# Performance work log

Hardware: AMD Instinct MI355X
Metric: run time of the kernel (lower is better)

Reference implementation:

```python
import jax, jax.numpy as jnp
import numpy as np

N_CENTER = 4000
N_NEIGH = 16
N_FEAT = 64
N_ATOMS = 20000
N_SPECIES = 8
COS_EPS = 1e-8  # torch cosine_similarity eps


def setup_inputs() -> dict:
    key = jax.random.key(0)
    k1, k2, k3, k4, k5, k6 = jax.random.split(key, 6)
    atom_i_idx = jax.random.randint(k1, (N_CENTER,), 0, N_ATOMS, dtype=jnp.int32)
    atom_j_idx = jax.random.randint(k2, (N_CENTER, N_NEIGH), 0, N_ATOMS, dtype=jnp.int32)
    # physical distances in [0.5, 4.5) Angstrom to avoid near-zero divisions
    dist_ij = jax.random.uniform(k3, (N_CENTER, N_NEIGH), dtype=jnp.float32) * 4.0 + 0.5
    atoms_xyz = jax.random.normal(k4, (N_ATOMS, 3), dtype=jnp.float32) * 5.0
    atoms_long = jax.random.randint(k5, (N_ATOMS, 2), 0, N_SPECIES, dtype=jnp.int32)
    embed_table = jax.random.normal(k6, (N_SPECIES, N_FEAT), dtype=jnp.float32)
    return {
        "nNeigh": N_NEIGH,
        "atom_i_idx": atom_i_idx,
        "atom_j_idx": atom_j_idx,
        "dist_ij": dist_ij,
        "atoms_xyz": atoms_xyz,
        "atoms_long": atoms_long,
        "embed_table": embed_table,
    }


def reference(nNeigh, atom_i_idx, atom_j_idx, dist_ij, atoms_xyz, atoms_long, embed_table):
    C = atom_i_idx.shape[0]
    N = nNeigh
    F = embed_table.shape[1]

    # --- triple geometry ---
    xyz_i = atoms_xyz[atom_i_idx][:, None, None, :]          # [C,1,1,3]
    xyz_j = atoms_xyz[atom_j_idx]                            # [C,N,3]
    vec_ij = xyz_j[:, :, None, :] - xyz_i                    # [C,N,1,3]
    vec_ik = xyz_j[:, None, :, :] - xyz_i                    # [C,1,N,3]

    dot = jnp.sum(vec_ij * vec_ik, axis=-1)                  # [C,N,N]
    norm_j = jnp.linalg.norm(vec_ij, axis=-1)                # [C,N,1]
    norm_k = jnp.linalg.norm(vec_ik, axis=-1)                # [C,1,N]
    cos = dot / (jnp.maximum(norm_j, COS_EPS) * jnp.maximum(norm_k, COS_EPS))
    ang = jnp.arccos(cos * 0.9999)                           # [C,N,N]

    d_ij = dist_ij[:, :, None, None]                         # [C,N,1,1]
    d_ik = dist_ij[:, None, :, None]                         # [C,1,N,1]

    # --- embeddings ---
    emb_i = embed_table[atoms_long[atom_i_idx, 1]]           # [C,F]
    emb_j = embed_table[atoms_long[atom_j_idx, 1]]           # [C,N,F]

    shp1 = (C, N, N, 1)
    shpF = (C, N, N, F)
    ang_desc = jnp.concatenate(
        (
            jnp.broadcast_to(d_ij, shp1),
            jnp.broadcast_to(d_ik, shp1),
            ang[..., None],
            jnp.broadcast_to(emb_i[:, None, None, :], shpF),
            jnp.broadcast_to(emb_j[:, :, None, :] / d_ij, shpF),
            jnp.broadcast_to(emb_j[:, None, :, :] / d_ik, shpF),
        ),
        axis=-1,
    )                                                         # [C,N,N,3+3F]

    # off-diagonal (j != k) triples, static index set
    jj, kk = np.nonzero(~np.eye(N, dtype=bool))
    ang_desc = ang_desc[:, jj, kk, :]                         # [C,N*(N-1),3+3F]
    return atom_i_idx.reshape(-1), ang_desc
```

## Files before the change

kernel.cpp:

```cpp
#include <hip/hip_runtime.h>
#include <math.h>

#define NNEI   16
#define NFEAT  64
#define NPAIR  240
#define ROWW   195
#define PER_C  (NPAIR * ROWW)
#define COS_EPS 1e-8f

typedef float f32x4 __attribute__((ext_vector_type(4)));

__device__ __host__ __forceinline__ int swz(int w) { return w ^ ((w >> 5) & 3); }

__global__ __launch_bounds__(256) void build_offtable(unsigned short* __restrict__ tab) {
    const int t = blockIdx.x * 256 + threadIdx.x;
    if (t >= PER_C) return;
    const unsigned p = (unsigned)t / 195u;
    const int s = t - (int)p * 195;
    const unsigned ju = p / 15u;
    const int j = (int)ju;
    const int r = (int)(p - ju * 15u);
    const int k = r + (r >= j);
    const int off =
          (s >= 131) ? (336 + (k << 6) + (s - 131))
        : (s >= 67)  ? (336 + (j << 6) + (s - 67))
        : (s >= 3)   ? (269 + s)
        : (s == 2)   ? ((j << 4) + k)
        : (s == 1)   ? (256 + k)
                     : (256 + j);
    tab[t] = (unsigned short)swz(off);
}

__global__ __launch_bounds__(256) void angdesc_kernel(
    const int*   __restrict__ atom_i_idx,
    const int*   __restrict__ atom_j_idx,
    const float* __restrict__ dist_ij,
    const float* __restrict__ atoms_xyz,
    const int*   __restrict__ atoms_long,
    const float* __restrict__ embed_table,
    const unsigned short* __restrict__ tab,
    float*       __restrict__ out0,
    float*       __restrict__ out1)
{
    __shared__ float s_lds[1360];
    __shared__ float s_vec[NNEI][3];
    __shared__ float s_nrm[NNEI];
    __shared__ float s_invd[NNEI];
    __shared__ int   s_spec[NNEI];

    const int c   = blockIdx.x;
    const int tid = threadIdx.x;
    const int ii  = atom_i_idx[c];

    if (tid == 0) out0[c] = (float)ii;

    const float xi = atoms_xyz[ii * 3 + 0];
    const float yi = atoms_xyz[ii * 3 + 1];
    const float zi = atoms_xyz[ii * 3 + 2];

    if (tid < NNEI) {
        const int jn = atom_j_idx[c * NNEI + tid];
        const float vx = atoms_xyz[jn * 3 + 0] - xi;
        const float vy = atoms_xyz[jn * 3 + 1] - yi;
        const float vz = atoms_xyz[jn * 3 + 2] - zi;
        s_vec[tid][0] = vx; s_vec[tid][1] = vy; s_vec[tid][2] = vz;
        s_nrm[tid]  = sqrtf(vx * vx + vy * vy + vz * vz);
        const float d = dist_ij[c * NNEI + tid];
        s_lds[swz(256 + tid)] = d;
        s_invd[tid] = 1.0f / d;
        s_spec[tid] = atoms_long[jn * 2 + 1];
    } else if (tid >= 64 && tid < 128) {
        const int f = tid - 64;
        const int speci = atoms_long[ii * 2 + 1];
        s_lds[swz(272 + f)] = embed_table[speci * NFEAT + f];
    }
    __syncthreads();

    {
        const int j = tid >> 4, k = tid & 15;
        const float dot = s_vec[j][0] * s_vec[k][0]
                        + s_vec[j][1] * s_vec[k][1]
                        + s_vec[j][2] * s_vec[k][2];
        const float nj = fmaxf(s_nrm[j], COS_EPS);
        const float nk = fmaxf(s_nrm[k], COS_EPS);
        const float cosv = dot / (nj * nk);
        s_lds[swz(tid)] = acosf(cosv * 0.9999f);
    }
    for (int e = tid; e < NNEI * NFEAT; e += 256) {
        const int n = e >> 6, f = e & 63;
        s_lds[swz(336 + e)] = embed_table[s_spec[n] * NFEAT + f] * s_invd[n];
    }
    __syncthreads();

    f32x4* __restrict__ dst4 = (f32x4*)(out1 + (size_t)c * PER_C);
    const ushort4* __restrict__ tab4 = (const ushort4*)tab;
    #pragma unroll 4
    for (int q = tid; q < PER_C / 4; q += 256) {
        const ushort4 o = tab4[q];
        f32x4 v;
        v.x = s_lds[o.x];
        v.y = s_lds[o.y];
        v.z = s_lds[o.z];
        v.w = s_lds[o.w];
        __builtin_nontemporal_store(v, dst4 + q);
    }
}

extern "C" void kernel_launch(void* const* d_in, const int* in_sizes, int n_in,
                              void* d_out, int out_size, void* d_ws, size_t ws_size,
                              hipStream_t stream) {
    const int*   atom_i_idx  = (const int*)  d_in[1];
    const int*   atom_j_idx  = (const int*)  d_in[2];
    const float* dist_ij     = (const float*)d_in[3];
    const float* atoms_xyz   = (const float*)d_in[4];
    const int*   atoms_long  = (const int*)  d_in[5];
    const float* embed_table = (const float*)d_in[6];

    const int C = in_sizes[1];
    float* out  = (float*)d_out;
    unsigned short* tab = (unsigned short*)d_ws;

    build_offtable<<<(PER_C + 255) / 256, 256, 0, stream>>>(tab);
    angdesc_kernel<<<C, 256, 0, stream>>>(atom_i_idx, atom_j_idx, dist_ij,
                                          atoms_xyz, atoms_long, embed_table,
                                          tab, out, out + C);
}
```

Before: 754.6 us.

## Make angular descriptor kernel persistent with multiple centers per block

Launches a fixed grid of 512 blocks, each processing 8 consecutive centers, with an XCD-interleaved block-to-work mapping. This amortizes block launch overhead and reuses the table across centers. It adds a fallback path that computes gather offsets inline when no workspace is available. In exchange it reduces the number of resident blocks and serializes each block's setup phase against its streaming stores, which may lower the parallelism available to hide latency.

Result: no change. 758.6 us (+0.5%).

```diff
diff --git a/kernel.cpp b/kernel.cpp
--- a/kernel.cpp
+++ b/kernel.cpp
@@ -6,7 +6,10 @@
 #define NPAIR  240
 #define ROWW   195
 #define PER_C  (NPAIR * ROWW)
+#define IMG    1360
 #define COS_EPS 1e-8f
+#define CPB    8
+#define NBLK   512
 
 typedef float f32x4 __attribute__((ext_vector_type(4)));
 
@@ -31,7 +34,23 @@
     tab[t] = (unsigned short)swz(off);
 }
 
-__global__ __launch_bounds__(256) void angdesc_kernel(
+__device__ __forceinline__ int off_of(int p, int s) {
+    const unsigned ju = (unsigned)p / 15u;
+    const int j = (int)ju;
+    const int r = p - (int)ju * 15;
+    const int k = r + (r >= j);
+    int off;
+    if      (s >= 131) off = 336 + (k << 6) + (s - 131);
+    else if (s >= 67)  off = 336 + (j << 6) + (s - 67);
+    else if (s >= 3)   off = 269 + s;
+    else if (s == 2)   off = (j << 4) + k;
+    else if (s == 1)   off = 256 + k;
+    else               off = 256 + j;
+    return swz(off);
+}
+
+template <bool USE_TAB>
+__global__ __launch_bounds__(256) void angdesc_persist(
     const int*   __restrict__ atom_i_idx,
     const int*   __restrict__ atom_j_idx,
     const float* __restrict__ dist_ij,
@@ -40,69 +59,92 @@
     const float* __restrict__ embed_table,
     const unsigned short* __restrict__ tab,
     float*       __restrict__ out0,
-    float*       __restrict__ out1)
+    float*       __restrict__ out1,
+    int C)
 {
-    __shared__ float s_lds[1360];
+    alignas(16) __shared__ float s_lds[IMG];
     __shared__ float s_vec[NNEI][3];
     __shared__ float s_nrm[NNEI];
     __shared__ float s_invd[NNEI];
     __shared__ int   s_spec[NNEI];
 
-    const int c   = blockIdx.x;
     const int tid = threadIdx.x;
-    const int ii  = atom_i_idx[c];
+    const int b = blockIdx.x;
+    const int logical = ((b & 7) << 6) + (b >> 3);
+    const int c0 = logical * CPB;
 
-    if (tid == 0) out0[c] = (float)ii;
+    for (int c = c0; c < c0 + CPB && c < C; ++c) {
+        __syncthreads();
 
-    const float xi = atoms_xyz[ii * 3 + 0];
-    const float yi = atoms_xyz[ii * 3 + 1];
-    const float zi = atoms_xyz[ii * 3 + 2];
+        const int ii = atom_i_idx[c];
+        if (tid == 0) out0[c] = (float)ii;
+        const float xi = atoms_xyz[ii * 3 + 0];
+        const float yi = atoms_xyz[ii * 3 + 1];
+        const float zi = atoms_xyz[ii * 3 + 2];
 
-    if (tid < NNEI) {
-        const int jn = atom_j_idx[c * NNEI + tid];
-        const float vx = atoms_xyz[jn * 3 + 0] - xi;
-        const float vy = atoms_xyz[jn * 3 + 1] - yi;
-        const float vz = atoms_xyz[jn * 3 + 2] - zi;
-        s_vec[tid][0] = vx; s_vec[tid][1] = vy; s_vec[tid][2] = vz;
-        s_nrm[tid]  = sqrtf(vx * vx + vy * vy + vz * vz);
-        const float d = dist_ij[c * NNEI + tid];
-        s_lds[swz(256 + tid)] = d;
-        s_invd[tid] = 1.0f / d;
-        s_spec[tid] = atoms_long[jn * 2 + 1];
-    } else if (tid >= 64 && tid < 128) {
-        const int f = tid - 64;
-        const int speci = atoms_long[ii * 2 + 1];
-        s_lds[swz(272 + f)] = embed_table[speci * NFEAT + f];
-    }
-    __syncthreads();
+        if (tid < NNEI) {
+            const int jn = atom_j_idx[c * NNEI + tid];
+            const float vx = atoms_xyz[jn * 3 + 0] - xi;
+            const float vy = atoms_xyz[jn * 3 + 1] - yi;
+            const float vz = atoms_xyz[jn * 3 + 2] - zi;
+            s_vec[tid][0] = vx; s_vec[tid][1] = vy; s_vec[tid][2] = vz;
+            s_nrm[tid]  = sqrtf(vx * vx + vy * vy + vz * vz);
+            const float d = dist_ij[c * NNEI + tid];
+            s_lds[swz(256 + tid)] = d;
+            s_invd[tid] = 1.0f / d;
+            s_spec[tid] = atoms_long[jn * 2 + 1];
+        } else if (tid >= 64 && tid < 128) {
+            const int f = tid - 64;
+            const int speci = atoms_long[ii * 2 + 1];
+            s_lds[swz(272 + f)] = embed_table[speci * NFEAT + f];
+        }
+        __syncthreads();
 
-    {
-        const int j = tid >> 4, k = tid & 15;
-        const float dot = s_vec[j][0] * s_vec[k][0]
-                        + s_vec[j][1] * s_vec[k][1]
-                        + s_vec[j][2] * s_vec[k][2];
-        const float nj = fmaxf(s_nrm[j], COS_EPS);
-        const float nk = fmaxf(s_nrm[k], COS_EPS);
-        const float cosv = dot / (nj * nk);
-        s_lds[swz(tid)] = acosf(cosv * 0.9999f);
-    }
-    for (int e = tid; e < NNEI * NFEAT; e += 256) {
-        const int n = e >> 6, f = e & 63;
-        s_lds[swz(336 + e)] = embed_table[s_spec[n] * NFEAT + f] * s_invd[n];
-    }
-    __syncthreads();
+        {
+            const int j = tid >> 4, k = tid & 15;
+            const float dot = s_vec[j][0] * s_vec[k][0]
+                            + s_vec[j][1] * s_vec[k][1]
+                            + s_vec[j][2] * s_vec[k][2];
+            const float nj = fmaxf(s_nrm[j], COS_EPS);
+            const float nk = fmaxf(s_nrm[k], COS_EPS);
+            s_lds[swz(tid)] = acosf((dot / (nj * nk)) * 0.9999f);
+        }
+        for (int e = tid; e < NNEI * NFEAT; e += 256) {
+            const int n = e >> 6, f = e & 63;
+            s_lds[swz(336 + e)] = embed_table[s_spec[n] * NFEAT + f] * s_invd[n];
+        }
+        __syncthreads();
 
-    f32x4* __restrict__ dst4 = (f32x4*)(out1 + (size_t)c * PER_C);
-    const ushort4* __restrict__ tab4 = (const ushort4*)tab;
-    #pragma unroll 4
-    for (int q = tid; q < PER_C / 4; q += 256) {
-        const ushort4 o = tab4[q];
-        f32x4 v;
-        v.x = s_lds[o.x];
-        v.y = s_lds[o.y];
-        v.z = s_lds[o.z];
-        v.w = s_lds[o.w];
-        __builtin_nontemporal_store(v, dst4 + q);
+        f32x4* __restrict__ dst4 = (f32x4*)(out1 + (size_t)c * PER_C);
+        if constexpr (USE_TAB) {
+            const ushort4* __restrict__ tab4 = (const ushort4*)tab;
+            #pragma unroll 2
+            for (int q = tid; q < PER_C / 4; q += 256) {
+                const ushort4 o = tab4[q];
+                f32x4 v;
+                v.x = s_lds[o.x];
+                v.y = s_lds[o.y];
+                v.z = s_lds[o.z];
+                v.w = s_lds[o.w];
+                __builtin_nontemporal_store(v, dst4 + q);
+            }
+        } else {
+            int p = (tid << 2) / 195;
+            int s = (tid << 2) - p * 195;
+            #pragma unroll 2
+            for (int q = tid; q < PER_C / 4; q += 256) {
+                f32x4 v;
+                #pragma unroll
+                for (int i = 0; i < 4; ++i) {
+                    int pp = p, ss = s + i;
+                    if (ss >= 195) { pp += 1; ss -= 195; }
+                    v[i] = s_lds[off_of(pp, ss)];
+                }
+                __builtin_nontemporal_store(v, dst4 + q);
+                s += 49; p += 5;
+                if (s >= 195) { s -= 195; p += 1; }
+            }
+        }
     }
 }
 
@@ -118,10 +160,17 @@
 
     const int C = in_sizes[1];
     float* out  = (float*)d_out;
-    unsigned short* tab = (unsigned short*)d_ws;
 
-    build_offtable<<<(PER_C + 255) / 256, 256, 0, stream>>>(tab);
-    angdesc_kernel<<<C, 256, 0, stream>>>(atom_i_idx, atom_j_idx, dist_ij,
-                                          atoms_xyz, atoms_long, embed_table,
-                                          tab, out, out + C);
+    const size_t need = (size_t)PER_C * sizeof(unsigned short);
+    if (d_ws != nullptr && ws_size >= need) {
+        unsigned short* tab = (unsigned short*)d_ws;
+        build_offtable<<<(PER_C + 255) / 256, 256, 0, stream>>>(tab);
+        angdesc_persist<true><<<NBLK, 256, 0, stream>>>(
+            atom_i_idx, atom_j_idx, dist_ij, atoms_xyz, atoms_long,
+            embed_table, tab, out, out + C, C);
+    } else {
+        angdesc_persist<false><<<NBLK, 256, 0, stream>>>(
+            atom_i_idx, atom_j_idx, dist_ij, atoms_xyz, atoms_long,
+            embed_table, nullptr, out, out + C, C);
+    }
 }
```
